# Kernel optimization log

Hardware: AMD Instinct MI355X
Metric: run time of the kernel (lower is better)

## Reference

```python
import jax, jax.numpy as jnp
import numpy as np

N = 65536
D_IN = 784
H = 20
D_OUT = 10
N_MID = 28  # fc2..fc29, all Linear(20,20)


def setup_inputs() -> dict:
    key = jax.random.key(0)
    ks = jax.random.split(key, 8)
    # PyTorch Linear default init: U(-1/sqrt(fan_in), 1/sqrt(fan_in)); uniform is fine for a reference.
    def uni(k, shape, fan_in):
        bound = 1.0 / np.sqrt(fan_in)
        return jax.random.uniform(k, shape, jnp.float32, -bound, bound)
    x = jax.random.normal(ks[0], (N, D_IN), jnp.float32)
    W1 = uni(ks[1], (H, D_IN), D_IN)
    b1 = uni(ks[2], (H,), D_IN)
    Wmid = uni(ks[3], (N_MID, H, H), H)   # stacked fc2..fc29 weights
    bmid = uni(ks[4], (N_MID, H), H)
    W30 = uni(ks[5], (D_OUT, H), H)
    b30 = uni(ks[6], (D_OUT,), H)
    return {"x": x, "W1": W1, "b1": b1, "Wmid": Wmid, "bmid": bmid, "W30": W30, "b30": b30}


def reference(x, W1, b1, Wmid, bmid, W30, b30):
    # fc1 + relu
    h = jax.nn.relu(x @ W1.T + b1)  # [N, 20]
    # fc2..fc29 + relu, identical structure -> scan over stacked params
    def step(h, wb):
        W, b = wb
        return jax.nn.relu(h @ W.T + b), None
    h, _ = jax.lax.scan(step, h, (Wmid, bmid))
    # fc30 (no relu)
    return h @ W30.T + b30  # [N, 10]
```

## Files before the change

kernel.cpp:

```cpp
#include <hip/hip_runtime.h>

typedef __attribute__((ext_vector_type(8))) short short8;
typedef __attribute__((ext_vector_type(16))) float f32x16;
typedef unsigned short ushort_t;

#define MFMA(A, B, C) __builtin_amdgcn_mfma_f32_32x32x16_bf16(A, B, C, 0, 0, 0)

__device__ __forceinline__ float4 ldf4(const float* p) { return *(const float4*)p; }
__device__ __forceinline__ short8 ld8(const void* p) { return *(const short8*)p; }

__device__ __forceinline__ short8 mk8(unsigned w0, unsigned w1, unsigned w2, unsigned w3) {
    union { unsigned u[4]; short8 s; } t;
    t.u[0] = w0; t.u[1] = w1; t.u[2] = w2; t.u[3] = w3;
    return t.s;
}
__device__ __forceinline__ unsigned packhi2(float a, float b) {
    return __builtin_amdgcn_perm(__float_as_uint(b), __float_as_uint(a), 0x07060302u);
}
__device__ __forceinline__ float lopart(float v) {
    return v - __uint_as_float(__float_as_uint(v) & 0xFFFF0000u);
}
__device__ __forceinline__ void plswap(unsigned& lo, unsigned& hi) {
    asm("v_permlane32_swap_b32 %0, %1" : "+v"(lo), "+v"(hi));
}
__device__ __forceinline__ ushort_t h16(float x) { return (ushort_t)(__float_as_uint(x) >> 16); }
__device__ __forceinline__ float fh(ushort_t u) { return __uint_as_float(((unsigned)u) << 16); }

__device__ __forceinline__ void dma16(const float* g, void* l) {
    __builtin_amdgcn_global_load_lds((const __attribute__((address_space(1))) void*)g,
                                     (__attribute__((address_space(3))) void*)l, 16, 0, 0);
}

__global__ void prepack(const float* __restrict__ W1,
                        const float* __restrict__ Wmid, const float* __restrict__ bmid,
                        const float* __restrict__ W30, const float* __restrict__ b30,
                        ushort_t* __restrict__ w1t, ushort_t* __restrict__ midt)
{
    const int tid = blockIdx.x * 256 + threadIdx.x;
    const int nth = gridDim.x * 256;
    for (int i = tid; i < 49 * 512; i += nth) {
        const int j = i & 7, hf = (i >> 3) & 1, o = (i >> 4) & 31, s = i >> 9;
        const float v = (o < 20) ? W1[o * 784 + s * 16 + hf * 8 + j] : 0.f;
        w1t[i] = h16(v);
    }
    for (int e2 = tid; e2 < 29 * 64; e2 += nth) {
        const int ee = e2 & 63, l = e2 >> 6;
        const int o = ee & 31, hf = ee >> 5;
        ushort_t v[32];
#pragma unroll
        for (int i = 0; i < 32; ++i) v[i] = 0;
        const bool lastl = (l == 28);
        const int omax = lastl ? 10 : 20;
        if (o < omax) {
            const float* wr = lastl ? (W30 + o * 20) : (Wmid + l * 400 + o * 20);
            const float bias = lastl ? b30[o] : bmid[l * 20 + o];
#pragma unroll
            for (int j = 0; j < 8; ++j) {
                const float w = wr[hf * 8 + j];
                v[j]      = h16(w);
                v[16 + j] = h16(w - fh(h16(w)));
            }
            if (hf == 0) {
#pragma unroll
                for (int j = 0; j < 4; ++j) {
                    const float w = wr[16 + j];
                    v[8 + j]  = h16(w);
                    v[24 + j] = h16(w - fh(h16(w)));
                }
                v[12] = h16(bias);
                v[13] = h16(bias - fh(h16(bias)));
            }
        }
#pragma unroll
        for (int f = 0; f < 4; ++f)
#pragma unroll
            for (int j = 0; j < 8; ++j)
                midt[l * 2048 + f * 512 + ee * 8 + j] = v[f * 8 + j];
    }
}

__global__ __launch_bounds__(256, 2)
void mlp_main(const float* __restrict__ x, const float* __restrict__ b1,
              const ushort_t* __restrict__ w1t, const ushort_t* __restrict__ midt,
              float* __restrict__ out, int nrows)
{
    __shared__ float xt[2][8192];
    __shared__ float xtail[2048];

    const int tid  = threadIdx.x;
    const int lane = tid & 63;
    const int wv   = tid >> 6;
    const int r0   = blockIdx.x * 128;
    if (r0 >= nrows) return;
    const int colr = lane & 31;
    const int half = lane >> 5;
    const int rowl = wv * 32 + colr;
    const int rsw  = rowl & 7;
    const int row  = r0 + rowl;

#define ISSUE_PHASE(PH, BUF) do {                                          \
        char* _lb = (char*)&xt[(BUF)][0] + (wv * 8) * 1024;                \
        const int _pc = (PH) * 64;                                         \
        _Pragma("unroll")                                                  \
        for (int k = 0; k < 8; ++k) {                                      \
            const int slot = (wv * 8 + k) * 64 + lane;                     \
            const int r = slot >> 4, gs = slot & 15;                       \
            const int g = gs ^ (r & 7);                                    \
            const size_t gr = (size_t)((r0 + r < nrows) ? (r0 + r) : (nrows - 1)); \
            dma16(x + gr * 784 + _pc + g * 4, _lb + k * 1024);             \
        }                                                                  \
    } while (0)

#pragma unroll
    for (int k = 0; k < 2; ++k) {
        const int slot = (wv * 2 + k) * 64 + lane;
        const int r = slot >> 2, u = slot & 3;
        const size_t gr = (size_t)((r0 + r < nrows) ? (r0 + r) : (nrows - 1));
        dma16(x + gr * 784 + 768 + u * 4, (char*)xtail + (wv * 2 + k) * 1024);
    }
    ISSUE_PHASE(0, 0);

    f32x16 acc;
#pragma unroll
    for (int r = 0; r < 16; ++r) acc[r] = 0.f;

#pragma unroll 1
    for (int p = 0; p < 12; ++p) {
        const ushort_t* ab = w1t + (p * 4) * 512 + colr * 16 + half * 8;
        const short8 A0 = ld8(ab);
        const short8 A1 = ld8(ab + 512);
        const short8 A2 = ld8(ab + 1024);
        const short8 A3 = ld8(ab + 1536);

        if (p < 11) {
            ISSUE_PHASE(p + 1, (p + 1) & 1);
            asm volatile("s_waitcnt vmcnt(8)" ::: "memory");
        } else {
            asm volatile("s_waitcnt vmcnt(0)" ::: "memory");
        }
        __builtin_amdgcn_sched_barrier(0);
        asm volatile("s_barrier" ::: "memory");
        __builtin_amdgcn_sched_barrier(0);

        const float* xl = &xt[p & 1][0];
#pragma unroll
        for (int s = 0; s < 4; ++s) {
            const int g = s * 4 + half * 2;
            const float4 va = *(const float4*)&xl[(rowl * 16 + (g ^ rsw)) * 4];
            const float4 vb = *(const float4*)&xl[(rowl * 16 + ((g + 1) ^ rsw)) * 4];
            const short8 B = mk8(packhi2(va.x, va.y), packhi2(va.z, va.w),
                                 packhi2(vb.x, vb.y), packhi2(vb.z, vb.w));
            acc = MFMA(s == 0 ? A0 : s == 1 ? A1 : s == 2 ? A2 : A3, B, acc);
        }
        asm volatile("s_barrier" ::: "memory");
    }

    {
        const short8 At = ld8(w1t + 48 * 512 + colr * 16 + half * 8);
        const float4 va = *(const float4*)&xtail[(rowl * 4 + half * 2) * 4];
        const float4 vb = *(const float4*)&xtail[(rowl * 4 + half * 2 + 1) * 4];
        const short8 B = mk8(packhi2(va.x, va.y), packhi2(va.z, va.w),
                             packhi2(vb.x, vb.y), packhi2(vb.z, vb.w));
        acc = MFMA(At, B, acc);
    }

    float Hv[16];
#pragma unroll
    for (int r = 0; r < 16; ++r) {
        const int o = (r & 3) + 8 * (r >> 2) + 4 * half;
        Hv[r] = fmaxf(acc[r] + b1[o < 20 ? o : 0], 0.f);
    }

    const ushort_t* ap = midt + lane * 8;
#pragma unroll 1
    for (int l = 0; l < 29; ++l) {
        const short8 A0h = ld8(ap + l * 2048);
        const short8 A1h = ld8(ap + l * 2048 + 512);
        const short8 A0l = ld8(ap + l * 2048 + 1024);
        const short8 A1l = ld8(ap + l * 2048 + 1536);

        unsigned plo0 = packhi2(Hv[0], Hv[1]), plo1 = packhi2(Hv[2], Hv[3]);
        unsigned phi0 = packhi2(Hv[4], Hv[5]), phi1 = packhi2(Hv[6], Hv[7]);
        plswap(plo0, phi0); plswap(plo1, phi1);
        const short8 B0h = mk8(plo0, plo1, phi0, phi1);

        unsigned qlo0 = packhi2(lopart(Hv[0]), lopart(Hv[1]));
        unsigned qlo1 = packhi2(lopart(Hv[2]), lopart(Hv[3]));
        unsigned qhi0 = packhi2(lopart(Hv[4]), lopart(Hv[5]));
        unsigned qhi1 = packhi2(lopart(Hv[6]), lopart(Hv[7]));
        plswap(qlo0, qhi0); plswap(qlo1, qhi1);
        const short8 B0l = mk8(qlo0, qlo1, qhi0, qhi1);

        const short8 B1h = mk8(half ? 0u : packhi2(Hv[8], Hv[9]),
                               half ? 0u : packhi2(Hv[10], Hv[11]),
                               half ? 0u : 0x00003F80u, 0u);
        const short8 B1l = mk8(half ? 0u : packhi2(lopart(Hv[8]), lopart(Hv[9])),
                               half ? 0u : packhi2(lopart(Hv[10]), lopart(Hv[11])),
                               half ? 0u : 0x3F800000u, 0u);

        f32x16 d;
#pragma unroll
        for (int r = 0; r < 16; ++r) d[r] = 0.f;
        d = MFMA(A0h, B0h, d);
        d = MFMA(A0l, B0h, d);
        d = MFMA(A0h, B0l, d);
        d = MFMA(A1h, B1h, d);
        d = MFMA(A1l, B1h, d);
        d = MFMA(A1h, B1l, d);

        if (l < 28) {
#pragma unroll
            for (int r = 0; r < 16; ++r) Hv[r] = fmaxf(d[r], 0.f);
        } else {
            if (row < nrows) {
#pragma unroll
                for (int r = 0; r < 16; ++r) {
                    const int o = (r & 3) + 8 * (r >> 2) + 4 * half;
                    if (o < 10) out[(size_t)row * 10 + o] = d[r];
                }
            }
        }
    }
#undef ISSUE_PHASE
}

extern "C" void kernel_launch(void* const* d_in, const int* in_sizes, int n_in,
                              void* d_out, int out_size, void* d_ws, size_t ws_size,
                              hipStream_t stream)
{
    const float* x    = (const float*)d_in[0];
    const float* W1   = (const float*)d_in[1];
    const float* b1   = (const float*)d_in[2];
    const float* Wmid = (const float*)d_in[3];
    const float* bmid = (const float*)d_in[4];
    const float* W30  = (const float*)d_in[5];
    const float* b30  = (const float*)d_in[6];
    float* out = (float*)d_out;

    ushort_t* w1t  = (ushort_t*)d_ws;
    ushort_t* midt = (ushort_t*)((char*)d_ws + 50176);

    const int nrows = in_sizes[0] / 784;
    prepack<<<32, 256, 0, stream>>>(W1, Wmid, bmid, W30, b30, w1t, midt);
    const int grid = (nrows + 127) / 128;
    mlp_main<<<grid, 256, 0, stream>>>(x, b1, w1t, midt, out, nrows);
}
```

Measured before the change: 52.63 us.

## Make x staging wave-private with smaller phases to drop barriers and raise occupancy

Each wave now DMAs only its own 32 rows of x into a private LDS region. That removes the workgroup s_barriers around every phase, since each wave consumes only what it loaded. Phase width is halved to 32 columns over 24 iterations, which halves the LDS buffer, and launch bounds go from 2 to 4 blocks per SM to allow more resident workgroups. The cost is more loop iterations with fewer loads in flight per phase, plus a tighter register budget. Without a barrier, correctness depends on vmcnt waits alone covering each wave's own LDS DMA writes.

```diff
diff --git a/kernel.cpp b/kernel.cpp
--- a/kernel.cpp
+++ b/kernel.cpp
@@ -79,12 +79,12 @@
     }
 }
 
-__global__ __launch_bounds__(256, 2)
+__global__ __launch_bounds__(256, 4)
 void mlp_main(const float* __restrict__ x, const float* __restrict__ b1,
               const ushort_t* __restrict__ w1t, const ushort_t* __restrict__ midt,
               float* __restrict__ out, int nrows)
 {
-    __shared__ float xt[2][8192];
+    __shared__ float xt[2][4096];
     __shared__ float xtail[2048];
 
     const int tid  = threadIdx.x;
@@ -94,29 +94,29 @@
     if (r0 >= nrows) return;
     const int colr = lane & 31;
     const int half = lane >> 5;
-    const int rowl = wv * 32 + colr;
-    const int rsw  = rowl & 7;
-    const int row  = r0 + rowl;
+    const int rsw  = colr & 7;
+    const int row  = r0 + wv * 32 + colr;
+    const int rw0  = r0 + wv * 32;
 
 #define ISSUE_PHASE(PH, BUF) do {                                          \
-        char* _lb = (char*)&xt[(BUF)][0] + (wv * 8) * 1024;                \
-        const int _pc = (PH) * 64;                                         \
+        char* _lb = (char*)&xt[(BUF)][wv * 1024];                          \
+        const int _pc = (PH) * 32;                                         \
         _Pragma("unroll")                                                  \
-        for (int k = 0; k < 8; ++k) {                                      \
-            const int slot = (wv * 8 + k) * 64 + lane;                     \
-            const int r = slot >> 4, gs = slot & 15;                       \
-            const int g = gs ^ (r & 7);                                    \
-            const size_t gr = (size_t)((r0 + r < nrows) ? (r0 + r) : (nrows - 1)); \
+        for (int k = 0; k < 4; ++k) {                                      \
+            const int slot = k * 64 + lane;                    \
+            const int rl = slot >> 3, gs = slot & 7;                       \
+            const int g = gs ^ (rl & 7);                                   \
+            const size_t gr = (size_t)((rw0 + rl < nrows) ? (rw0 + rl) : (nrows - 1)); \
             dma16(x + gr * 784 + _pc + g * 4, _lb + k * 1024);             \
         }                                                                  \
     } while (0)
 
 #pragma unroll
     for (int k = 0; k < 2; ++k) {
-        const int slot = (wv * 2 + k) * 64 + lane;
-        const int r = slot >> 2, u = slot & 3;
-        const size_t gr = (size_t)((r0 + r < nrows) ? (r0 + r) : (nrows - 1));
-        dma16(x + gr * 784 + 768 + u * 4, (char*)xtail + (wv * 2 + k) * 1024);
+        const int slot = k * 64 + lane;
+        const int rl = slot >> 2, u = slot & 3;
+        const size_t gr = (size_t)((rw0 + rl < nrows) ? (rw0 + rl) : (nrows - 1));
+        dma16(x + gr * 784 + 768 + u * 4, (char*)xtail + wv * 2048 + k * 1024);
     }
     ISSUE_PHASE(0, 0);
 
@@ -125,40 +125,36 @@
     for (int r = 0; r < 16; ++r) acc[r] = 0.f;
 
 #pragma unroll 1
-    for (int p = 0; p < 12; ++p) {
-        const ushort_t* ab = w1t + (p * 4) * 512 + colr * 16 + half * 8;
+    for (int p = 0; p < 24; ++p) {
+        const ushort_t* ab = w1t + (p * 2) * 512 + colr * 16 + half * 8;
         const short8 A0 = ld8(ab);
         const short8 A1 = ld8(ab + 512);
-        const short8 A2 = ld8(ab + 1024);
-        const short8 A3 = ld8(ab + 1536);
-
-        if (p < 11) {
+
+        if (p < 23) {
             ISSUE_PHASE(p + 1, (p + 1) & 1);
-            asm volatile("s_waitcnt vmcnt(8)" ::: "memory");
+            asm volatile("s_waitcnt vmcnt(4)" ::: "memory");
         } else {
             asm volatile("s_waitcnt vmcnt(0)" ::: "memory");
         }
         __builtin_amdgcn_sched_barrier(0);
-        asm volatile("s_barrier" ::: "memory");
-        __builtin_amdgcn_sched_barrier(0);
-
-        const float* xl = &xt[p & 1][0];
-#pragma unroll
-        for (int s = 0; s < 4; ++s) {
+
+        const float* xl = &xt[p & 1][wv * 1024 + colr * 32];
+#pragma unroll
+        for (int s = 0; s < 2; ++s) {
             const int g = s * 4 + half * 2;
-            const float4 va = *(const float4*)&xl[(rowl * 16 + (g ^ rsw)) * 4];
-            const float4 vb = *(const float4*)&xl[(rowl * 16 + ((g + 1) ^ rsw)) * 4];
+            const float4 va = *(const float4*)&xl[((g)     ^ rsw) * 4];
+            const float4 vb = *(const float4*)&xl[((g + 1) ^ rsw) * 4];
             const short8 B = mk8(packhi2(va.x, va.y), packhi2(va.z, va.w),
                                  packhi2(vb.x, vb.y), packhi2(vb.z, vb.w));
-            acc = MFMA(s == 0 ? A0 : s == 1 ? A1 : s == 2 ? A2 : A3, B, acc);
-        }
-        asm volatile("s_barrier" ::: "memory");
+            acc = MFMA(s == 0 ? A0 : A1, B, acc);
+        }
     }
 
     {
         const short8 At = ld8(w1t + 48 * 512 + colr * 16 + half * 8);
-        const float4 va = *(const float4*)&xtail[(rowl * 4 + half * 2) * 4];
-        const float4 vb = *(const float4*)&xtail[(rowl * 4 + half * 2 + 1) * 4];
+        const float* tl = &xtail[wv * 512 + colr * 16];
+        const float4 va = ldf4(&tl[(half * 2) * 4]);
+        const float4 vb = ldf4(&tl[(half * 2 + 1) * 4]);
         const short8 B = mk8(packhi2(va.x, va.y), packhi2(va.z, va.w),
                              packhi2(vb.x, vb.y), packhi2(vb.z, vb.w));
         acc = MFMA(At, B, acc);
```

New measurement: 52.07 us. No clear change (-1.1%).
